# Optimization experiments

Measured on AMD Instinct MI355X. Metric: run time of the kernel, lower is better.

The kernel has to match this reference:

```python
import jax, jax.numpy as jnp
import numpy as np

DIM = 768
HEADS = 8
HEAD_DIM = DIM // HEADS
SCALE = DIM ** (-0.5)  # faithful: original scales by dimension**-0.5, not head_dim


def setup_inputs() -> dict:
    key = jax.random.key(0)
    k1, k2, k3 = jax.random.split(key, 3)
    B, N = 2, 4096
    x = jax.random.normal(k1, (B, N, DIM), dtype=jnp.float32)
    # qkv projection params (Linear(dim, 3*dim))
    W_qkv = jax.random.normal(k2, (DIM, 3 * DIM), dtype=jnp.float32) * (DIM ** -0.5)
    b_qkv = jax.random.normal(k3, (3 * DIM,), dtype=jnp.float32) * 0.01
    return {"x": x, "W_qkv": W_qkv, "b_qkv": b_qkv}


def reference(x, W_qkv, b_qkv):
    B, N, D = x.shape
    qkv = x @ W_qkv + b_qkv                       # (B, N, 3D)
    qkv = qkv.reshape(B, N, 3, HEADS, HEAD_DIM)
    q, k, v = jnp.moveaxis(qkv, 2, 0)             # each (B, N, H, dh)
    # (B, H, N, N) scores — explicit materialization as in the source
    scores = jnp.einsum('bnhd,bmhd->bhnm', q, k) * SCALE
    attn = jax.nn.softmax(scores, axis=-1)
    out = jnp.einsum('bhnm,bmhd->bnhd', attn, v)  # (B, N, H, dh)
    return out.reshape(B, N, D)
```

## Files before the change

kernel.cpp:

```cpp
#include <hip/hip_runtime.h>
#include <hip/hip_bf16.h>


typedef __attribute__((ext_vector_type(8)))  short    bf16x8;
typedef __attribute__((ext_vector_type(4)))  float    floatx4;
typedef __attribute__((ext_vector_type(16))) float    floatx16;
typedef __attribute__((ext_vector_type(8)))  unsigned short us8;
typedef __attribute__((ext_vector_type(4)))  unsigned short us4;

#define HEADS 8
#define DH 96
#define NSEQ 4096
#define DIM 768
#define SCALE2_F (0.03608439182435161f * 1.4426950408889634f)

__device__ __forceinline__ unsigned short f2bf(float f) {
    union { float f; unsigned u; } v; v.f = f;
    unsigned r = v.u + 0x7fffu + ((v.u >> 16) & 1u);
    return (unsigned short)(r >> 16);
}

__device__ __forceinline__ unsigned pk2(float a, float b) {
    float2 t; t.x = a; t.y = b;
    __hip_bfloat162 r = __float22bfloat162_rn(t);
    return *(unsigned*)&r;
}

__device__ __forceinline__ bf16x8 mk_pfrag(float c0, float c1, float c2, float c3,
                                           float c4, float c5, float c6, float c7, int hB) {
    unsigned pl0 = pk2(c0, c1), pl1 = pk2(c2, c3);
    unsigned pu0 = pk2(c4, c5), pu1 = pk2(c6, c7);
    unsigned s0 = hB ? pl0 : pu0, s1 = hB ? pl1 : pu1;
    unsigned r0 = (unsigned)__shfl_xor((int)s0, 32);
    unsigned r1 = (unsigned)__shfl_xor((int)s1, 32);
    union { unsigned u[4]; bf16x8 v; } f;
    f.u[0] = hB ? r0 : pl0;
    f.u[1] = hB ? r1 : pl1;
    f.u[2] = hB ? pu0 : r0;
    f.u[3] = hB ? pu1 : r1;
    return f.v;
}

__global__ __launch_bounds__(256) void cvt_x(const float* __restrict__ x, unsigned short* __restrict__ xb) {
    int i = blockIdx.x * 256 + threadIdx.x;
    float4 v = ((const float4*)x)[i];
    us4 o; o.x = f2bf(v.x); o.y = f2bf(v.y); o.z = f2bf(v.z); o.w = f2bf(v.w);
    ((us4*)xb)[i] = o;
}

__global__ __launch_bounds__(256) void cvt_w(const float* __restrict__ w, unsigned short* __restrict__ wt) {
    __shared__ unsigned short sm[64][33];
    int c0 = blockIdx.x * 32, k0 = blockIdx.y * 64;
    int t = threadIdx.x;
    int cl = t & 31, kl0 = t >> 5;
    for (int i = 0; i < 8; ++i) {
        int kl = kl0 + i * 8;
        sm[kl][cl] = f2bf(w[(k0 + kl) * 2304 + c0 + cl]);
    }
    __syncthreads();
    int kl2 = t & 63, cl0 = t >> 6;
    for (int i = 0; i < 8; ++i) {
        int cl2 = cl0 + i * 4;
        wt[(c0 + cl2) * 768 + k0 + kl2] = sm[kl2][cl2];
    }
}

__global__ __launch_bounds__(256) void gemm_qkv(const unsigned short* __restrict__ xb,
                                                const unsigned short* __restrict__ wt,
                                                const float* __restrict__ bias,
                                                unsigned short* __restrict__ qb,
                                                unsigned short* __restrict__ kb,
                                                unsigned short* __restrict__ vt) {
    __shared__ unsigned short As[128 * 72];
    __shared__ unsigned short Bs[128 * 72];
    const int tid = threadIdx.x;
    const int lane = tid & 63, wv = tid >> 6;
    const int n15 = lane & 15, quad = lane >> 4;
    const int m0 = blockIdx.y * 128, c0 = blockIdx.x * 128;
    const int mw = (wv >> 1) * 64, nw = (wv & 1) * 64;
    floatx4 acc[4][4] = {};

    for (int kt = 0; kt < 12; ++kt) {
        for (int i = 0; i < 4; ++i) {
            int g = i * 256 + tid;
            int row = g >> 3, gc = g & 7;
            *(us8*)&As[row * 72 + gc * 8] = *(const us8*)&xb[(m0 + row) * 768 + kt * 64 + gc * 8];
            *(us8*)&Bs[row * 72 + gc * 8] = *(const us8*)&wt[(c0 + row) * 768 + kt * 64 + gc * 8];
        }
        __syncthreads();
        for (int ks = 0; ks < 2; ++ks) {
            bf16x8 af[4], bfr[4];
            for (int mt = 0; mt < 4; ++mt)
                af[mt] = *(const bf16x8*)&As[(mw + mt * 16 + n15) * 72 + ks * 32 + quad * 8];
            for (int nt = 0; nt < 4; ++nt)
                bfr[nt] = *(const bf16x8*)&Bs[(nw + nt * 16 + n15) * 72 + ks * 32 + quad * 8];
            for (int mt = 0; mt < 4; ++mt)
                for (int nt = 0; nt < 4; ++nt)
                    acc[mt][nt] = __builtin_amdgcn_mfma_f32_16x16x32_bf16(af[mt], bfr[nt], acc[mt][nt], 0, 0, 0);
        }
        __syncthreads();
    }
    for (int nt = 0; nt < 4; ++nt) {
        int c = c0 + nw + nt * 16 + n15;
        float bv = bias[c];
        int which = c / 768, rem = c % 768;
        int h = rem / 96, d = rem % 96;
        for (int mt = 0; mt < 4; ++mt) {
            for (int r = 0; r < 4; ++r) {
                int m = m0 + mw + mt * 16 + quad * 4 + r;
                int b = m >> 12, n = m & 4095;
                float val = acc[mt][nt][r] + bv;
                int bh = b * HEADS + h;
                if (which == 0)      qb[(bh * NSEQ + n) * DH + d] = f2bf(val * SCALE2_F);
                else if (which == 1) kb[(bh * NSEQ + n) * DH + d] = f2bf(val);
                else                 vt[(bh * DH + d) * NSEQ + n] = f2bf(val);
            }
        }
    }
}

__global__ __launch_bounds__(256, 2) void flash(const unsigned short* __restrict__ qb,
                                                const unsigned short* __restrict__ kb,
                                                const unsigned short* __restrict__ vt,
                                                float* __restrict__ out) {
    __shared__ unsigned short sm[28672];
    __shared__ float l_all[128];

    const int tid = threadIdx.x;
    const int lane = tid & 63, wv = tid >> 6;
    const int l31 = lane & 31, h = lane >> 5;
    const int x7 = l31 & 7;
    const int id = blockIdx.x;
    const int bh = id & 15;
    const int q0 = (id >> 4) * 128 + wv * 32;

    const unsigned short* kgb = kb + (size_t)bh * NSEQ * DH;
    const unsigned short* vgb = vt + (size_t)bh * DH * NSEQ;

    bf16x8 qf[6];
    {
        const unsigned short* qrow = qb + (size_t)(bh * NSEQ + q0 + l31) * DH;
#pragma unroll
        for (int ks = 0; ks < 6; ++ks)
            qf[ks] = *(const bf16x8*)&qrow[ks * 16 + h * 8];
    }

    int kofs[2][6];
#pragma unroll
    for (int kt = 0; kt < 2; ++kt)
#pragma unroll
        for (int ks = 0; ks < 6; ++ks) {
            int b = 2 * ks + h;
            int bs = (b < 8) ? (b ^ x7) : (8 + ((b - 8) ^ x7));
            kofs[kt][ks] = (kt * 32 + l31) * 128 + bs * 8;
        }
    int vofs[3][4];
#pragma unroll
    for (int dt = 0; dt < 3; ++dt)
#pragma unroll
        for (int s = 0; s < 4; ++s)
            vofs[dt][s] = (dt * 32 + l31) * 64 + ((2 * s + h) ^ x7) * 8;

    int goffk[3], goffv[3], wofk[3], wofv[3];
#pragma unroll
    for (int i = 0; i < 3; ++i) {
        int tb = i * 256 + tid;
        int r = tb / 12, bb = tb % 12;
        goffk[i] = r * 96 + bb * 8;
        int bs = (bb < 8) ? (bb ^ (r & 7)) : (8 + ((bb - 8) ^ (r & 7)));
        wofk[i] = r * 128 + bs * 8;
        int d = tb >> 3, b2 = tb & 7;
        goffv[i] = d * 4096 + b2 * 8;
        wofv[i] = d * 64 + ((b2 ^ (d & 7))) * 8;
    }

    us8 kr[3], vr[3];
    const unsigned short* kpf = kgb;
    const unsigned short* vpf = vgb;
#pragma unroll
    for (int i = 0; i < 3; ++i) { kr[i] = *(const us8*)&kpf[goffk[i]]; vr[i] = *(const us8*)&vpf[goffv[i]]; }
    kpf += 6144; vpf += 64;
#pragma unroll
    for (int i = 0; i < 3; ++i) { *(us8*)&sm[wofk[i]] = kr[i]; *(us8*)&sm[16384 + wofv[i]] = vr[i]; }
#pragma unroll
    for (int i = 0; i < 3; ++i) { kr[i] = *(const us8*)&kpf[goffk[i]]; vr[i] = *(const us8*)&vpf[goffv[i]]; }
    kpf += 6144; vpf += 64;
    __syncthreads();

    floatx16 stA[2] = {}, stB[2] = {};
#pragma unroll
    for (int ks = 0; ks < 6; ++ks)
#pragma unroll
        for (int kt = 0; kt < 2; ++kt) {
            bf16x8 ak = *(const bf16x8*)&sm[kofs[kt][ks]];
            stA[kt] = __builtin_amdgcn_mfma_f32_32x32x16_bf16(ak, qf[ks], stA[kt], 0, 0, 0);
        }

    floatx16 o[3] = {};
    float lsum = 0.f;

    auto body = [&](int kv, floatx16 (&cur)[2], floatx16 (&nxt)[2]) {
        const int nb = (kv + 1) & 1, cb = kv & 1;
        if (kv < 63) {
            unsigned short* Kd = sm + nb * 8192;
            unsigned short* Vd = sm + 16384 + nb * 6144;
#pragma unroll
            for (int i = 0; i < 3; ++i) { *(us8*)&Kd[wofk[i]] = kr[i]; *(us8*)&Vd[wofv[i]] = vr[i]; }
            if (kv < 62) {
#pragma unroll
                for (int i = 0; i < 3; ++i) { kr[i] = *(const us8*)&kpf[goffk[i]]; vr[i] = *(const us8*)&vpf[goffv[i]]; }
                kpf += 6144; vpf += 64;
            }
        }
        __syncthreads();

        const unsigned short* Kn = sm + nb * 8192;
        const unsigned short* Vc = sm + 16384 + cb * 6144;

        if (kv < 63) {
#pragma unroll
            for (int ks = 0; ks < 6; ++ks)
#pragma unroll
                for (int kt = 0; kt < 2; ++kt) {
                    bf16x8 ak = *(const bf16x8*)&Kn[kofs[kt][ks]];
                    nxt[kt] = __builtin_amdgcn_mfma_f32_32x32x16_bf16(ak, qf[ks], nxt[kt], 0, 0, 0);
                }
        }

#pragma unroll
        for (int kt = 0; kt < 2; ++kt)
#pragma unroll
            for (int rg = 0; rg < 16; ++rg) {
                float p = __builtin_amdgcn_exp2f(cur[kt][rg]);
                cur[kt][rg] = p;
                lsum += p;
            }
        bf16x8 pf[4];
        pf[0] = mk_pfrag(cur[0][0], cur[0][1], cur[0][2], cur[0][3],
                         cur[0][4], cur[0][5], cur[0][6], cur[0][7], h);
        pf[1] = mk_pfrag(cur[0][8], cur[0][9], cur[0][10], cur[0][11],
                         cur[0][12], cur[0][13], cur[0][14], cur[0][15], h);
        pf[2] = mk_pfrag(cur[1][0], cur[1][1], cur[1][2], cur[1][3],
                         cur[1][4], cur[1][5], cur[1][6], cur[1][7], h);
        pf[3] = mk_pfrag(cur[1][8], cur[1][9], cur[1][10], cur[1][11],
                         cur[1][12], cur[1][13], cur[1][14], cur[1][15], h);
#pragma unroll
        for (int kt = 0; kt < 2; ++kt)
            cur[kt] = (floatx16)(0.f);

#pragma unroll
        for (int s = 0; s < 4; ++s)
#pragma unroll
            for (int dt = 0; dt < 3; ++dt) {
                bf16x8 bv = *(const bf16x8*)&Vc[vofs[dt][s]];
                o[dt] = __builtin_amdgcn_mfma_f32_32x32x16_bf16(pf[s], bv, o[dt], 0, 0, 0);
            }

        __syncthreads();
    };

    for (int kv = 0; kv < 64; kv += 2) {
        body(kv, stA, stB);
        body(kv + 1, stB, stA);
    }

    lsum += __shfl_xor(lsum, 32);
    if (h == 0) l_all[wv * 32 + l31] = lsum;
    __syncthreads();

    const int b = bh >> 3, hd = bh & 7;
#pragma unroll
    for (int rg = 0; rg < 16; ++rg) {
        int row = (rg & 3) + 8 * (rg >> 2) + 4 * h;
        float inv = 1.0f / l_all[wv * 32 + row];
        int q = q0 + row;
        float* op = out + (size_t)(b * NSEQ + q) * DIM + hd * DH;
#pragma unroll
        for (int dt = 0; dt < 3; ++dt)
            op[dt * 32 + l31] = o[dt][rg] * inv;
    }
}

extern "C" void kernel_launch(void* const* d_in, const int* in_sizes, int n_in,
                              void* d_out, int out_size, void* d_ws, size_t ws_size,
                              hipStream_t stream) {
    const float* x    = (const float*)d_in[0];
    const float* W    = (const float*)d_in[1];
    const float* bias = (const float*)d_in[2];
    float* out = (float*)d_out;

    char* ws = (char*)d_ws;
    unsigned short* xb = (unsigned short*)(ws);
    unsigned short* wt = (unsigned short*)(ws + 12582912);
    unsigned short* qb = (unsigned short*)(ws + 16121856);
    unsigned short* kb = (unsigned short*)(ws + 28704768);
    unsigned short* vt = (unsigned short*)(ws + 41287680);

    cvt_x<<<6144, 256, 0, stream>>>(x, xb);
    cvt_w<<<dim3(72, 12), 256, 0, stream>>>(W, wt);
    gemm_qkv<<<dim3(18, 64), 256, 0, stream>>>(xb, wt, bias, qb, kb, vt);
    flash<<<512, 256, 0, stream>>>(qb, kb, vt, out);
}
```

Baseline: 259.1 us.

## Split V projection into transposed GEMM and triple-buffer V to drop barrier

The QKV projection is split into two kernels. One writes Q and K. The other computes V with the operands swapped, so each thread's stores to the transposed V layout run along the sequence dimension and coalesce, instead of scattering stride-4096 writes. In the flash kernel, the V tile buffer goes from double to triple buffering, which lets the trailing __syncthreads of each iteration be removed. The QK^T accumulators are now initialised through a zero operand on the first MFMA instead of an explicit zeroing loop. These changes cost an extra kernel launch and more shared memory per block, which could reduce occupancy at two blocks per CU.

Result: faster. 250.7 us (-3.3%).

```diff
diff --git a/kernel.cpp b/kernel.cpp
--- a/kernel.cpp
+++ b/kernel.cpp
@@ -65,12 +65,11 @@
     }
 }
 
-__global__ __launch_bounds__(256) void gemm_qkv(const unsigned short* __restrict__ xb,
-                                                const unsigned short* __restrict__ wt,
-                                                const float* __restrict__ bias,
-                                                unsigned short* __restrict__ qb,
-                                                unsigned short* __restrict__ kb,
-                                                unsigned short* __restrict__ vt) {
+__global__ __launch_bounds__(256) void gemm_qk(const unsigned short* __restrict__ xb,
+                                               const unsigned short* __restrict__ wt,
+                                               const float* __restrict__ bias,
+                                               unsigned short* __restrict__ qb,
+                                               unsigned short* __restrict__ kb) {
     __shared__ unsigned short As[128 * 72];
     __shared__ unsigned short Bs[128 * 72];
     const int tid = threadIdx.x;
@@ -111,9 +110,55 @@
                 int b = m >> 12, n = m & 4095;
                 float val = acc[mt][nt][r] + bv;
                 int bh = b * HEADS + h;
-                if (which == 0)      qb[(bh * NSEQ + n) * DH + d] = f2bf(val * SCALE2_F);
-                else if (which == 1) kb[(bh * NSEQ + n) * DH + d] = f2bf(val);
-                else                 vt[(bh * DH + d) * NSEQ + n] = f2bf(val);
+                if (which == 0) qb[(bh * NSEQ + n) * DH + d] = f2bf(val * SCALE2_F);
+                else            kb[(bh * NSEQ + n) * DH + d] = f2bf(val);
+            }
+        }
+    }
+}
+
+__global__ __launch_bounds__(256) void gemm_v(const unsigned short* __restrict__ xb,
+                                              const unsigned short* __restrict__ wt,
+                                              const float* __restrict__ bias,
+                                              unsigned short* __restrict__ vt) {
+    __shared__ unsigned short As[128 * 72];
+    __shared__ unsigned short Bs[128 * 72];
+    const int tid = threadIdx.x;
+    const int lane = tid & 63, wv = tid >> 6;
+    const int n15 = lane & 15, quad = lane >> 4;
+    const int m0 = blockIdx.y * 128, c0 = blockIdx.x * 128;
+    const int mw = (wv >> 1) * 64, nw = (wv & 1) * 64;
+    floatx4 acc[4][4] = {};
+
+    for (int kt = 0; kt < 12; ++kt) {
+        for (int i = 0; i < 4; ++i) {
+            int g = i * 256 + tid;
+            int row = g >> 3, gc = g & 7;
+            *(us8*)&As[row * 72 + gc * 8] = *(const us8*)&wt[(1536 + m0 + row) * 768 + kt * 64 + gc * 8];
+            *(us8*)&Bs[row * 72 + gc * 8] = *(const us8*)&xb[(c0 + row) * 768 + kt * 64 + gc * 8];
+        }
+        __syncthreads();
+        for (int ks = 0; ks < 2; ++ks) {
+            bf16x8 af[4], bfr[4];
+            for (int mt = 0; mt < 4; ++mt)
+                af[mt] = *(const bf16x8*)&As[(mw + mt * 16 + n15) * 72 + ks * 32 + quad * 8];
+            for (int nt = 0; nt < 4; ++nt)
+                bfr[nt] = *(const bf16x8*)&Bs[(nw + nt * 16 + n15) * 72 + ks * 32 + quad * 8];
+            for (int mt = 0; mt < 4; ++mt)
+                for (int nt = 0; nt < 4; ++nt)
+                    acc[mt][nt] = __builtin_amdgcn_mfma_f32_16x16x32_bf16(af[mt], bfr[nt], acc[mt][nt], 0, 0, 0);
+        }
+        __syncthreads();
+    }
+    for (int mt = 0; mt < 4; ++mt) {
+        for (int r = 0; r < 4; ++r) {
+            int dv = m0 + mw + mt * 16 + quad * 4 + r;
+            float bv = bias[1536 + dv];
+            int h = dv / 96, d = dv % 96;
+            for (int nt = 0; nt < 4; ++nt) {
+                int ng = c0 + nw + nt * 16 + n15;
+                int b = ng >> 12, n = ng & 4095;
+                vt[((size_t)(b * HEADS + h) * DH + d) * NSEQ + n] = f2bf(acc[mt][nt][r] + bv);
             }
         }
     }
@@ -123,7 +168,7 @@
                                                 const unsigned short* __restrict__ kb,
                                                 const unsigned short* __restrict__ vt,
                                                 float* __restrict__ out) {
-    __shared__ unsigned short sm[28672];
+    __shared__ unsigned short sm[34816];
     __shared__ float l_all[128];
 
     const int tid = threadIdx.x;
@@ -174,6 +219,8 @@
         wofv[i] = d * 64 + ((b2 ^ (d & 7))) * 8;
     }
 
+    const floatx16 z16 = (floatx16)(0.f);
+
     us8 kr[3], vr[3];
     const unsigned short* kpf = kgb;
     const unsigned short* vpf = vgb;
@@ -187,23 +234,22 @@
     kpf += 6144; vpf += 64;
     __syncthreads();
 
-    floatx16 stA[2] = {}, stB[2] = {};
+    floatx16 stA[2], stB[2];
 #pragma unroll
     for (int ks = 0; ks < 6; ++ks)
 #pragma unroll
         for (int kt = 0; kt < 2; ++kt) {
             bf16x8 ak = *(const bf16x8*)&sm[kofs[kt][ks]];
-            stA[kt] = __builtin_amdgcn_mfma_f32_32x32x16_bf16(ak, qf[ks], stA[kt], 0, 0, 0);
+            stA[kt] = __builtin_amdgcn_mfma_f32_32x32x16_bf16(ak, qf[ks], ks == 0 ? z16 : stA[kt], 0, 0, 0);
         }
 
     floatx16 o[3] = {};
     float lsum = 0.f;
 
     auto body = [&](int kv, floatx16 (&cur)[2], floatx16 (&nxt)[2]) {
-        const int nb = (kv + 1) & 1, cb = kv & 1;
         if (kv < 63) {
-            unsigned short* Kd = sm + nb * 8192;
-            unsigned short* Vd = sm + 16384 + nb * 6144;
+            unsigned short* Kd = sm + ((kv + 1) & 1) * 8192;
+            unsigned short* Vd = sm + 16384 + ((kv + 1) % 3) * 6144;
 #pragma unroll
             for (int i = 0; i < 3; ++i) { *(us8*)&Kd[wofk[i]] = kr[i]; *(us8*)&Vd[wofv[i]] = vr[i]; }
             if (kv < 62) {
@@ -214,16 +260,14 @@
         }
         __syncthreads();
 
-        const unsigned short* Kn = sm + nb * 8192;
-        const unsigned short* Vc = sm + 16384 + cb * 6144;
-
         if (kv < 63) {
+            const unsigned short* Kn = sm + ((kv + 1) & 1) * 8192;
 #pragma unroll
             for (int ks = 0; ks < 6; ++ks)
 #pragma unroll
                 for (int kt = 0; kt < 2; ++kt) {
                     bf16x8 ak = *(const bf16x8*)&Kn[kofs[kt][ks]];
-                    nxt[kt] = __builtin_amdgcn_mfma_f32_32x32x16_bf16(ak, qf[ks], nxt[kt], 0, 0, 0);
+                    nxt[kt] = __builtin_amdgcn_mfma_f32_32x32x16_bf16(ak, qf[ks], ks == 0 ? z16 : nxt[kt], 0, 0, 0);
                 }
         }
 
@@ -244,10 +288,8 @@
                          cur[1][4], cur[1][5], cur[1][6], cur[1][7], h);
         pf[3] = mk_pfrag(cur[1][8], cur[1][9], cur[1][10], cur[1][11],
                          cur[1][12], cur[1][13], cur[1][14], cur[1][15], h);
-#pragma unroll
-        for (int kt = 0; kt < 2; ++kt)
-            cur[kt] = (floatx16)(0.f);
-
+
+        const unsigned short* Vc = sm + 16384 + (kv % 3) * 6144;
 #pragma unroll
         for (int s = 0; s < 4; ++s)
 #pragma unroll
@@ -255,8 +297,6 @@
                 bf16x8 bv = *(const bf16x8*)&Vc[vofs[dt][s]];
                 o[dt] = __builtin_amdgcn_mfma_f32_32x32x16_bf16(pf[s], bv, o[dt], 0, 0, 0);
             }
-
-        __syncthreads();
     };
 
     for (int kv = 0; kv < 64; kv += 2) {
@@ -298,6 +338,7 @@
 
     cvt_x<<<6144, 256, 0, stream>>>(x, xb);
     cvt_w<<<dim3(72, 12), 256, 0, stream>>>(W, wt);
-    gemm_qkv<<<dim3(18, 64), 256, 0, stream>>>(xb, wt, bias, qb, kb, vt);
+    gemm_qk<<<dim3(12, 64), 256, 0, stream>>>(xb, wt, bias, qb, kb);
+    gemm_v<<<dim3(64, 6), 256, 0, stream>>>(xb, wt, bias, vt);
     flash<<<512, 256, 0, stream>>>(qb, kb, vt, out);
 }
```
